# Performance work log

Measured on AMD Instinct MI355X. Metric: run time of the kernel, lower is better.

Reference implementation:

```python
import jax, jax.numpy as jnp
import numpy as np

N, E, D, H = 100000, 1000000, 64, 4
HD = D // H  # head dim
G = 64       # num graphs in batch
EPS = 1e-5
NEG_SLOPE = 0.2


def setup_inputs() -> dict:
    key = jax.random.key(0)
    ks = jax.random.split(key, 10)
    x = jax.random.normal(ks[0], (N, D), dtype=jnp.float32)
    edge_index = jax.random.randint(ks[1], (2, E), 0, N)
    batch = jnp.sort(jax.random.randint(ks[2], (N,), 0, G))
    s = 1.0 / np.sqrt(D)
    Wl = jax.random.uniform(ks[3], (D, D), jnp.float32, -s, s)   # lin_l (source)
    Wr = jax.random.uniform(ks[4], (D, D), jnp.float32, -s, s)   # lin_r (target)
    att = jax.random.uniform(ks[5], (H, HD), jnp.float32, -s, s)
    bias_gat = jnp.zeros((D,), jnp.float32)
    gn_weight = jnp.ones((D,), jnp.float32)
    gn_bias = jnp.zeros((D,), jnp.float32)
    gn_mean_scale = jnp.ones((D,), jnp.float32)
    return {"x": x, "edge_index": edge_index, "batch": batch, "Wl": Wl,
            "Wr": Wr, "att": att, "bias_gat": bias_gat, "gn_weight": gn_weight,
            "gn_bias": gn_bias, "gn_mean_scale": gn_mean_scale}


def _gatv2(x, src, dst, Wl, Wr, att, bias_gat):
    # per-node linear projections, reshaped to heads
    xl = (x @ Wl).reshape(N, H, HD)  # source features
    xr = (x @ Wr).reshape(N, H, HD)  # target features
    # per-edge attention logits: a^T LeakyReLU(xl_j + xr_i)
    e = xl[src] + xr[dst]                             # [E', H, HD]
    e = jnp.where(e >= 0, e, NEG_SLOPE * e)           # leaky_relu
    score = jnp.einsum('ehd,hd->eh', e, att)          # [E', H]
    # segment softmax over incoming edges of each dst node
    m = jax.ops.segment_max(score, dst, num_segments=N)   # [N, H]
    p = jnp.exp(score - m[dst])
    denom = jax.ops.segment_sum(p, dst, num_segments=N)   # [N, H]
    alpha = p / denom[dst]                                # [E', H]
    # weighted scatter-add aggregation of source features
    out = jax.ops.segment_sum(alpha[:, :, None] * xl[src], dst, num_segments=N)
    return out.reshape(N, D) + bias_gat


def _graph_norm(h, batch, weight, bias, mean_scale):
    cnt = jax.ops.segment_sum(jnp.ones((N,), h.dtype), batch, num_segments=G)
    cnt = jnp.maximum(cnt, 1.0)[:, None]                      # [G,1]
    mean = jax.ops.segment_sum(h, batch, num_segments=G) / cnt
    out = h - mean_scale * mean[batch]
    var = jax.ops.segment_sum(out * out, batch, num_segments=G) / cnt
    return weight * out / jnp.sqrt(var[batch] + EPS) + bias


def reference(x, edge_index, batch, Wl, Wr, att, bias_gat, gn_weight, gn_bias, gn_mean_scale):
    # eval mode: dropout / DropEdge are identity; pre_norm=False; res_proj=Identity
    loops = jnp.arange(N)
    src = jnp.concatenate([edge_index[0], loops])  # add self-loops (PyG default)
    dst = jnp.concatenate([edge_index[1], loops])
    h = _gatv2(x, src, dst, Wl, Wr, att, bias_gat)
    h = h + x                                       # identity residual
    h = jnp.where(h > 0, h, jnp.expm1(h))           # ELU
    h = _graph_norm(h, batch, gn_weight, gn_bias, gn_mean_scale)
    return h
```

## Files before the change

kernel.cpp:

```cpp
#include <hip/hip_runtime.h>
#include <hip/hip_bf16.h>
#include <math.h>

#define G_ 64
#define NEG_SLOPE 0.2f
#define EPS_ 1e-5f
#define BBITS 7
#define BSZ 128
#define CAP 2048
#define EPB 2048

typedef __attribute__((ext_vector_type(8))) unsigned short ushort8;
typedef __attribute__((ext_vector_type(8))) short bf16x8;
typedef __attribute__((ext_vector_type(4))) float f32x4;

#define DPP_ADD(t, ctrl)                                                   \
  do {                                                                     \
    int _p = __builtin_amdgcn_update_dpp(0, __float_as_int(t), (ctrl),     \
                                         0xf, 0xf, true);                  \
    (t) += __int_as_float(_p);                                             \
  } while (0)
#define REDUCE8(t)                                                         \
  do {                                                                     \
    DPP_ADD(t, 0xB1);                                                      \
    DPP_ADD(t, 0x4E);                                                      \
    DPP_ADD(t, 0x141);                                                     \
  } while (0)

__device__ __forceinline__ float leaky_(float e) {
  return 0.6f * e + 0.4f * fabsf(e);
}

__device__ __forceinline__ short f2bf(float f) {
  __hip_bfloat16 h = __float2bfloat16(f);
  return *reinterpret_cast<short*>(&h);
}

__global__ __launch_bounds__(256) void init_kernel(
    const float* __restrict__ Wl, const float* __restrict__ Wr,
    bf16x8* __restrict__ bpack, int* __restrict__ bcnt,
    float* __restrict__ gzero, int nb) {
  if (blockIdx.x == 0) {
    const int lane = threadIdx.x;
    if (lane < 64) {
      const int lrow = lane & 15;
      const int lgrp = lane >> 4;
#pragma unroll
      for (int ct = 0; ct < 8; ++ct) {
        const float* W = (ct < 4) ? Wl : Wr;
        const int col = ((ct & 3) * 16) + lrow;
#pragma unroll
        for (int kk = 0; kk < 2; ++kk) {
          const int kb = kk * 32 + lgrp * 8;
          bf16x8 f;
#pragma unroll
          for (int j = 0; j < 8; ++j) f[j] = f2bf(W[(kb + j) * 64 + col]);
          bpack[(ct * 2 + kk) * 64 + lane] = f;
        }
      }
    }
  } else {
    const int idx = (blockIdx.x - 1) * 256 + threadIdx.x;
    const int stride = (gridDim.x - 1) * 256;
    for (int j = idx; j < nb; j += stride) bcnt[j] = 0;
    for (int j = idx; j < 2 * G_ * 64 + G_; j += stride) gzero[j] = 0.f;
  }
}

__global__ __launch_bounds__(256) void projbucket_kernel(
    const float* __restrict__ x, const bf16x8* __restrict__ bpack,
    __hip_bfloat16* __restrict__ xlb, __hip_bfloat16* __restrict__ xrb,
    const int* __restrict__ esrc, const int* __restrict__ edst,
    int* __restrict__ bcnt, unsigned int* __restrict__ packed,
    int n, int e, int nb, int nbucket) {
  __shared__ int cnt[800];
  __shared__ int base[800];
  if ((int)blockIdx.x < nbucket) {
    const int t = threadIdx.x;
    const int e0 = blockIdx.x * EPB;
    const int e1 = (e0 + EPB) < e ? (e0 + EPB) : e;
    int dloc[8], sloc[8];
#pragma unroll
    for (int it = 0; it < 8; ++it) {
      const int i = e0 + t + it * 256;
      const bool ok = i < e1;
      dloc[it] = ok ? edst[i] : -1;
      sloc[it] = ok ? esrc[i] : 0;
    }
    for (int b = t; b < nb; b += 256) cnt[b] = 0;
    __syncthreads();
#pragma unroll
    for (int it = 0; it < 8; ++it)
      if (dloc[it] >= 0) atomicAdd(&cnt[dloc[it] >> BBITS], 1);
    __syncthreads();
    for (int b = t; b < nb; b += 256) {
      int c = cnt[b];
      base[b] = c ? atomicAdd(&bcnt[b], c) : 0;
      cnt[b] = 0;
    }
    __syncthreads();
#pragma unroll
    for (int it = 0; it < 8; ++it) {
      if (dloc[it] >= 0) {
        const int d = dloc[it];
        const int b = d >> BBITS;
        const int pos = base[b] + atomicAdd(&cnt[b], 1);
        if (pos < CAP)
          packed[(size_t)b * CAP + pos] =
              ((unsigned)(d & (BSZ - 1)) << 17) | (unsigned)sloc[it];
      }
    }
  } else {
    const int lane = threadIdx.x & 63;
    const int wv = threadIdx.x >> 6;
    const int rbase = (blockIdx.x - nbucket) * 64 + wv * 16;
    const int lrow = lane & 15;
    const int lgrp = lane >> 4;

    bf16x8 bfrag[8][2];
#pragma unroll
    for (int ct = 0; ct < 8; ++ct)
#pragma unroll
      for (int kk = 0; kk < 2; ++kk)
        bfrag[ct][kk] = bpack[(ct * 2 + kk) * 64 + lane];

    bf16x8 afrag[2];
    const int r = rbase + lrow;
#pragma unroll
    for (int kk = 0; kk < 2; ++kk) {
      bf16x8 f;
      if (r < n) {
        const float4* p =
            (const float4*)(x + (size_t)r * 64 + kk * 32 + lgrp * 8);
        float4 u = p[0], v = p[1];
        f[0] = f2bf(u.x); f[1] = f2bf(u.y); f[2] = f2bf(u.z); f[3] = f2bf(u.w);
        f[4] = f2bf(v.x); f[5] = f2bf(v.y); f[6] = f2bf(v.z); f[7] = f2bf(v.w);
      } else {
        f = bf16x8{0, 0, 0, 0, 0, 0, 0, 0};
      }
      afrag[kk] = f;
    }

    f32x4 acc[8];
#pragma unroll
    for (int ct = 0; ct < 8; ++ct) acc[ct] = f32x4{0.f, 0.f, 0.f, 0.f};
#pragma unroll
    for (int ct = 0; ct < 8; ++ct)
#pragma unroll
      for (int kk = 0; kk < 2; ++kk)
        acc[ct] = __builtin_amdgcn_mfma_f32_16x16x32_bf16(
            afrag[kk], bfrag[ct][kk], acc[ct], 0, 0, 0);

#pragma unroll
    for (int ct = 0; ct < 8; ++ct) {
      __hip_bfloat16* dst = (ct < 4) ? xlb : xrb;
      const int c = ((ct & 3) * 16) + lrow;
#pragma unroll
      for (int j = 0; j < 4; ++j) {
        const int rr = rbase + lgrp * 4 + j;
        if (rr < n) dst[(size_t)rr * 64 + c] = __float2bfloat16(acc[ct][j]);
      }
    }
  }
}

__global__ __launch_bounds__(256) void sort_kernel(
    unsigned int* __restrict__ packed, const int* __restrict__ bcnt,
    int2* __restrict__ nse, int n) {
  __shared__ unsigned int stage[CAP];
  __shared__ int cnt[BSZ];
  __shared__ int sc[BSZ];
  __shared__ int off[BSZ + 1];
  const int t = threadIdx.x;
  const int b = blockIdx.x;
  int ecnt = bcnt[b];
  if (ecnt > CAP) ecnt = CAP;
  for (int j = t; j < ecnt; j += 256) stage[j] = packed[(size_t)b * CAP + j];
  if (t < BSZ) cnt[t] = 0;
  __syncthreads();
  for (int j = t; j < ecnt; j += 256) atomicAdd(&cnt[stage[j] >> 17], 1);
  __syncthreads();
  if (t < BSZ) sc[t] = cnt[t];
  __syncthreads();
#pragma unroll
  for (int o = 1; o < BSZ; o <<= 1) {
    int v = 0;
    if (t < BSZ && t >= o) v = sc[t - o];
    __syncthreads();
    if (t < BSZ) sc[t] += v;
    __syncthreads();
  }
  if (t < BSZ) {
    off[t + 1] = sc[t];
    if (t == 0) off[0] = 0;
    cnt[t] = sc[t] - cnt[t];
  }
  __syncthreads();
  for (int j = t; j < ecnt; j += 256) {
    unsigned v = stage[j];
    int pos = atomicAdd(&cnt[v >> 17], 1);
    packed[(size_t)b * CAP + pos] = v & 0x1FFFF;
  }
  const int nodebase = b << BBITS;
  if (t < BSZ && nodebase + t < n) {
    int s = off[t];
    nse[nodebase + t] = make_int2(b * CAP + s, off[t + 1] - s);
  }
}

template <int NB>
__device__ __forceinline__ void burst_(
    const char* xbase, unsigned poff, int myedge, int half, int tot,
    float xr0, float xr1, float a0, float a1,
    float& acc0, float& acc1, float& den) {
  unsigned vv[NB];
#pragma unroll
  for (int j = 0; j < NB; ++j) {
    const int sa = __builtin_amdgcn_readlane(myedge, 2 * j);
    const int sb = __builtin_amdgcn_readlane(myedge, 2 * j + 1);
    const int s = half ? sb : sa;
    vv[j] = *(const unsigned*)(xbase + (((unsigned)s << 7) | poff));
  }
#pragma unroll
  for (int j = 0; j < NB; ++j) {
    const unsigned v = vv[j];
    const float l0 = __uint_as_float(v << 16);
    const float l1 = __uint_as_float(v & 0xFFFF0000u);
    float e0 = leaky_(l0 + xr0);
    float e1 = leaky_(l1 + xr1);
    float t = a0 * e0 + a1 * e1;
    REDUCE8(t);
    float p = exp2f(t);
    p = ((2 * j + half) < tot) ? p : 0.f;
    acc0 = fmaf(p, l0, acc0);
    acc1 = fmaf(p, l1, acc1);
    den += p;
  }
}

__global__ __launch_bounds__(256) void aggregate_kernel(
    const __hip_bfloat16* __restrict__ xlb,
    const __hip_bfloat16* __restrict__ xrb, const float* __restrict__ x,
    const float* __restrict__ att, const float* __restrict__ bias_gat,
    const int2* __restrict__ nse, const unsigned int* __restrict__ srt,
    __hip_bfloat16* __restrict__ hb, int n) {
  const int lane = threadIdx.x & 63;
  const int i = (blockIdx.x * blockDim.x + threadIdx.x) >> 6;
  if (i >= n) return;
  const int pos = lane & 31;
  const int half = lane >> 5;
  const float2 attp = ((const float2*)att)[pos];
  const float a0 = attp.x * 1.44269504f;
  const float a1 = attp.y * 1.44269504f;
  const unsigned xr_pk = ((const unsigned*)(xrb + (size_t)i * 64))[pos];
  const float xr0 = __uint_as_float(xr_pk << 16);
  const float xr1 = __uint_as_float(xr_pk & 0xFFFF0000u);
  int2 sd = nse[i];
  const int s0 = __builtin_amdgcn_readfirstlane(sd.x);
  const int deg = __builtin_amdgcn_readfirstlane(sd.y);
  const int tot = deg + 1;
  int myedge = i;
  if (lane > 0 && lane < tot) myedge = (int)srt[s0 + lane - 1];
  float acc0 = 0.f, acc1 = 0.f, den = 0.f;
  const char* xbase = (const char*)xlb;
  const unsigned poff = (unsigned)pos << 2;

  if (tot <= 8) {
    burst_<4>(xbase, poff, myedge, half, tot, xr0, xr1, a0, a1,
              acc0, acc1, den);
  } else {
    burst_<8>(xbase, poff, myedge, half, tot, xr0, xr1, a0, a1,
              acc0, acc1, den);
    const int kmax = tot < 64 ? tot : 64;
    for (int k = 16; k < kmax; k += 2) {
      const int sa = __builtin_amdgcn_readlane(myedge, k);
      const int sb = (k + 1 < kmax) ? __builtin_amdgcn_readlane(myedge, k + 1)
                                    : sa;
      const int s = half ? sb : sa;
      const unsigned v = *(const unsigned*)(xbase + (((unsigned)s << 7) | poff));
      const float l0 = __uint_as_float(v << 16);
      const float l1 = __uint_as_float(v & 0xFFFF0000u);
      float e0 = leaky_(l0 + xr0);
      float e1 = leaky_(l1 + xr1);
      float t = a0 * e0 + a1 * e1;
      REDUCE8(t);
      float p = exp2f(t);
      p = ((k + half) < kmax) ? p : 0.f;
      acc0 = fmaf(p, l0, acc0);
      acc1 = fmaf(p, l1, acc1);
      den += p;
    }
    for (int kk = 64; kk < tot; ++kk) {
      const int s = (int)srt[s0 + kk - 1];
      const unsigned v = *(const unsigned*)(xbase + (((unsigned)s << 7) | poff));
      const float l0 = __uint_as_float(v << 16);
      const float l1 = __uint_as_float(v & 0xFFFF0000u);
      float e0 = leaky_(l0 + xr0);
      float e1 = leaky_(l1 + xr1);
      float t = a0 * e0 + a1 * e1;
      REDUCE8(t);
      float p = exp2f(t);
      p = half ? 0.f : p;
      acc0 = fmaf(p, l0, acc0);
      acc1 = fmaf(p, l1, acc1);
      den += p;
    }
  }

  acc0 += __shfl_xor(acc0, 32);
  acc1 += __shfl_xor(acc1, 32);
  den += __shfl_xor(den, 32);
  if (half == 0) {
    const float inv = 1.f / den;
    const float2 xres = ((const float2*)(x + (size_t)i * 64))[pos];
    const float2 bb = ((const float2*)bias_gat)[pos];
    float h0 = fmaf(acc0, inv, bb.x) + xres.x;
    float h1 = fmaf(acc1, inv, bb.y) + xres.y;
    h0 = h0 > 0.f ? h0 : expm1f(h0);
    h1 = h1 > 0.f ? h1 : expm1f(h1);
    __hip_bfloat16 b0 = __float2bfloat16(h0);
    __hip_bfloat16 b1 = __float2bfloat16(h1);
    unsigned pk = ((unsigned)(*(unsigned short*)&b1) << 16) |
                  (unsigned)(*(unsigned short*)&b0);
    ((unsigned*)(hb + (size_t)i * 64))[pos] = pk;
  }
}

__global__ __launch_bounds__(256) void gsum2_kernel(
    const __hip_bfloat16* __restrict__ h, const int* __restrict__ batch,
    float* __restrict__ gsum, float* __restrict__ gsq,
    float* __restrict__ gcnt, int n) {
  const int lane = threadIdx.x & 63;
  const int wave = (blockIdx.x * blockDim.x + threadIdx.x) >> 6;
  const int nwaves = (gridDim.x * blockDim.x) >> 6;
  const int chunk = (n + nwaves - 1) / nwaves;
  const int start = wave * chunk;
  const int end = (start + chunk) < n ? (start + chunk) : n;
  float s1 = 0.f, s2 = 0.f, cntl = 0.f;
  int curg = -1;
  for (int i = start; i < end; ++i) {
    int g = batch[i];
    if (g != curg) {
      if (curg >= 0) {
        atomicAdd(&gsum[curg * 64 + lane], s1);
        atomicAdd(&gsq[curg * 64 + lane], s2);
        if (lane == 0) atomicAdd(&gcnt[curg], cntl);
      }
      curg = g; s1 = 0.f; s2 = 0.f; cntl = 0.f;
    }
    float hv = __bfloat162float(h[(size_t)i * 64 + lane]);
    s1 += hv;
    s2 += hv * hv;
    cntl += 1.f;
  }
  if (curg >= 0) {
    atomicAdd(&gsum[curg * 64 + lane], s1);
    atomicAdd(&gsq[curg * 64 + lane], s2);
    if (lane == 0) atomicAdd(&gcnt[curg], cntl);
  }
}

__global__ __launch_bounds__(256) void out_kernel(
    const __hip_bfloat16* __restrict__ hb, const int* __restrict__ batch,
    const float* __restrict__ gsum, const float* __restrict__ gsq,
    const float* __restrict__ gcnt, const float* __restrict__ mscale,
    const float* __restrict__ w, const float* __restrict__ bias,
    float* __restrict__ out, int n) {
  const int total8 = n * 8;
  for (int idx = blockIdx.x * blockDim.x + threadIdx.x; idx < total8;
       idx += gridDim.x * blockDim.x) {
    int i = idx >> 3, q = idx & 7;
    int g = batch[i];
    float c = gcnt[g];
    c = c > 1.f ? c : 1.f;
    float inv = 1.f / c;
    int base = g * 64 + q * 8;
    ushort8 hv8 = ((const ushort8*)hb)[idx];
    float r[8];
#pragma unroll
    for (int j = 0; j < 8; ++j) {
      int dd = q * 8 + j;
      float mean = gsum[base + j] * inv;
      float ms = mscale[dd];
      float var = gsq[base + j] * inv - ms * (2.f - ms) * mean * mean;
      float f = __uint_as_float(((unsigned)hv8[j]) << 16);
      r[j] = (f - ms * mean) * (w[dd] * rsqrtf(var + EPS_)) + bias[dd];
    }
    float4 o0 = make_float4(r[0], r[1], r[2], r[3]);
    float4 o1 = make_float4(r[4], r[5], r[6], r[7]);
    ((float4*)out)[idx * 2] = o0;
    ((float4*)out)[idx * 2 + 1] = o1;
  }
}

extern "C" void kernel_launch(void* const* d_in, const int* in_sizes, int n_in,
                              void* d_out, int out_size, void* d_ws, size_t ws_size,
                              hipStream_t stream) {
  const float* x        = (const float*)d_in[0];
  const int*   eidx     = (const int*)d_in[1];
  const int*   batch    = (const int*)d_in[2];
  const float* Wl       = (const float*)d_in[3];
  const float* Wr       = (const float*)d_in[4];
  const float* att      = (const float*)d_in[5];
  const float* bias_gat = (const float*)d_in[6];
  const float* gw       = (const float*)d_in[7];
  const float* gb       = (const float*)d_in[8];
  const float* gms      = (const float*)d_in[9];
  const int N = in_sizes[0] / 64;
  const int E = in_sizes[1] / 2;
  const int* esrc = eidx;
  const int* edst = eidx + E;
  float* out = (float*)d_out;
  const int NB_ = (N + BSZ - 1) >> BBITS;

  char* wsp = (char*)d_ws;
  float* gsum   = (float*)wsp;                wsp += G_ * 64 * 4;
  float* gsq    = (float*)wsp;                wsp += G_ * 64 * 4;
  float* gcnt   = (float*)wsp;                wsp += G_ * 4;
  bf16x8* bpack = (bf16x8*)wsp;               wsp += 16 * 64 * 16;
  int*   bcnt   = (int*)wsp;                  wsp += (size_t)NB_ * 4;
  int2*  nse    = (int2*)wsp;                 wsp += (size_t)N * 8;
  unsigned int* packed = (unsigned int*)wsp;  wsp += (size_t)NB_ * CAP * 4;
  __hip_bfloat16* xlb = (__hip_bfloat16*)wsp; wsp += (size_t)N * 64 * 2;
  __hip_bfloat16* xrb = (__hip_bfloat16*)wsp; wsp += (size_t)N * 64 * 2;
  __hip_bfloat16* hb  = (__hip_bfloat16*)wsp; wsp += (size_t)N * 64 * 2;

  init_kernel<<<9, 256, 0, stream>>>(Wl, Wr, bpack, bcnt, gsum, NB_);

  const int nbucket = (E + EPB - 1) / EPB;
  const int nproj = (N + 63) / 64;
  projbucket_kernel<<<nbucket + nproj, 256, 0, stream>>>(
      x, bpack, xlb, xrb, esrc, edst, bcnt, packed, N, E, NB_, nbucket);

  sort_kernel<<<NB_, 256, 0, stream>>>(packed, bcnt, nse, N);

  aggregate_kernel<<<(N + 3) / 4, 256, 0, stream>>>(
      xlb, xrb, x, att, bias_gat, nse, packed, hb, N);

  gsum2_kernel<<<1024, 256, 0, stream>>>(hb, batch, gsum, gsq, gcnt, N);
  out_kernel<<<3125, 256, 0, stream>>>(hb, batch, gsum, gsq, gcnt, gms, gw,
                                       gb, out, N);
}
```

Measured before the change: 153.9 us.

## Pair projection with sort kernel and store bf16 copy of x for residual

The edge-bucketing step becomes its own kernel, and the node projection GEMM now shares a launch with the per-bucket sort kernel instead of the bucketing kernel. This balances work across the two launches. The projection also writes a bf16 copy of x, so the aggregate kernel reads the residual at half the bytes instead of fp32 x. In exchange it adds an extra N×64 bf16 write and workspace buffer, and the residual is rounded to bf16 precision.

```diff
diff --git a/kernel.cpp b/kernel.cpp
--- a/kernel.cpp
+++ b/kernel.cpp
@@ -67,53 +67,98 @@
   }
 }
 
-__global__ __launch_bounds__(256) void projbucket_kernel(
-    const float* __restrict__ x, const bf16x8* __restrict__ bpack,
-    __hip_bfloat16* __restrict__ xlb, __hip_bfloat16* __restrict__ xrb,
+__global__ __launch_bounds__(256) void bucket_kernel(
     const int* __restrict__ esrc, const int* __restrict__ edst,
     int* __restrict__ bcnt, unsigned int* __restrict__ packed,
-    int n, int e, int nb, int nbucket) {
+    int e, int nb) {
   __shared__ int cnt[800];
   __shared__ int base[800];
-  if ((int)blockIdx.x < nbucket) {
+  const int t = threadIdx.x;
+  const int e0 = blockIdx.x * EPB;
+  const int e1 = (e0 + EPB) < e ? (e0 + EPB) : e;
+  int dloc[8], sloc[8];
+#pragma unroll
+  for (int it = 0; it < 8; ++it) {
+    const int i = e0 + t + it * 256;
+    const bool ok = i < e1;
+    dloc[it] = ok ? edst[i] : -1;
+    sloc[it] = ok ? esrc[i] : 0;
+  }
+  for (int b = t; b < nb; b += 256) cnt[b] = 0;
+  __syncthreads();
+#pragma unroll
+  for (int it = 0; it < 8; ++it)
+    if (dloc[it] >= 0) atomicAdd(&cnt[dloc[it] >> BBITS], 1);
+  __syncthreads();
+  for (int b = t; b < nb; b += 256) {
+    int c = cnt[b];
+    base[b] = c ? atomicAdd(&bcnt[b], c) : 0;
+    cnt[b] = 0;
+  }
+  __syncthreads();
+#pragma unroll
+  for (int it = 0; it < 8; ++it) {
+    if (dloc[it] >= 0) {
+      const int d = dloc[it];
+      const int b = d >> BBITS;
+      const int pos = base[b] + atomicAdd(&cnt[b], 1);
+      if (pos < CAP)
+        packed[(size_t)b * CAP + pos] =
+            ((unsigned)(d & (BSZ - 1)) << 17) | (unsigned)sloc[it];
+    }
+  }
+}
+
+__global__ __launch_bounds__(256) void sortproj_kernel(
+    unsigned int* __restrict__ packed, const int* __restrict__ bcnt,
+    int2* __restrict__ nse, const float* __restrict__ x,
+    const bf16x8* __restrict__ bpack, __hip_bfloat16* __restrict__ xlb,
+    __hip_bfloat16* __restrict__ xrb, __hip_bfloat16* __restrict__ xb,
+    int n, int nsort) {
+  __shared__ unsigned int stage[CAP];
+  __shared__ int cnt[BSZ];
+  __shared__ int sc[BSZ];
+  __shared__ int off[BSZ + 1];
+  if ((int)blockIdx.x < nsort) {
     const int t = threadIdx.x;
-    const int e0 = blockIdx.x * EPB;
-    const int e1 = (e0 + EPB) < e ? (e0 + EPB) : e;
-    int dloc[8], sloc[8];
-#pragma unroll
-    for (int it = 0; it < 8; ++it) {
-      const int i = e0 + t + it * 256;
-      const bool ok = i < e1;
-      dloc[it] = ok ? edst[i] : -1;
-      sloc[it] = ok ? esrc[i] : 0;
-    }
-    for (int b = t; b < nb; b += 256) cnt[b] = 0;
+    const int b = blockIdx.x;
+    int ecnt = bcnt[b];
+    if (ecnt > CAP) ecnt = CAP;
+    for (int j = t; j < ecnt; j += 256) stage[j] = packed[(size_t)b * CAP + j];
+    if (t < BSZ) cnt[t] = 0;
     __syncthreads();
-#pragma unroll
-    for (int it = 0; it < 8; ++it)
-      if (dloc[it] >= 0) atomicAdd(&cnt[dloc[it] >> BBITS], 1);
+    for (int j = t; j < ecnt; j += 256) atomicAdd(&cnt[stage[j] >> 17], 1);
     __syncthreads();
-    for (int b = t; b < nb; b += 256) {
-      int c = cnt[b];
-      base[b] = c ? atomicAdd(&bcnt[b], c) : 0;
-      cnt[b] = 0;
-    }
+    if (t < BSZ) sc[t] = cnt[t];
     __syncthreads();
 #pragma unroll
-    for (int it = 0; it < 8; ++it) {
-      if (dloc[it] >= 0) {
-        const int d = dloc[it];
-        const int b = d >> BBITS;
-        const int pos = base[b] + atomicAdd(&cnt[b], 1);
-        if (pos < CAP)
-          packed[(size_t)b * CAP + pos] =
-              ((unsigned)(d & (BSZ - 1)) << 17) | (unsigned)sloc[it];
-      }
+    for (int o = 1; o < BSZ; o <<= 1) {
+      int v = 0;
+      if (t < BSZ && t >= o) v = sc[t - o];
+      __syncthreads();
+      if (t < BSZ) sc[t] += v;
+      __syncthreads();
+    }
+    if (t < BSZ) {
+      off[t + 1] = sc[t];
+      if (t == 0) off[0] = 0;
+      cnt[t] = sc[t] - cnt[t];
+    }
+    __syncthreads();
+    for (int j = t; j < ecnt; j += 256) {
+      unsigned v = stage[j];
+      int pos = atomicAdd(&cnt[v >> 17], 1);
+      packed[(size_t)b * CAP + pos] = v & 0x1FFFF;
+    }
+    const int nodebase = b << BBITS;
+    if (t < BSZ && nodebase + t < n) {
+      int s = off[t];
+      nse[nodebase + t] = make_int2(b * CAP + s, off[t + 1] - s);
     }
   } else {
     const int lane = threadIdx.x & 63;
     const int wv = threadIdx.x >> 6;
-    const int rbase = (blockIdx.x - nbucket) * 64 + wv * 16;
+    const int rbase = (blockIdx.x - nsort) * 64 + wv * 16;
     const int lrow = lane & 15;
     const int lgrp = lane >> 4;
 
@@ -135,6 +180,7 @@
         float4 u = p[0], v = p[1];
         f[0] = f2bf(u.x); f[1] = f2bf(u.y); f[2] = f2bf(u.z); f[3] = f2bf(u.w);
         f[4] = f2bf(v.x); f[5] = f2bf(v.y); f[6] = f2bf(v.z); f[7] = f2bf(v.w);
+        *reinterpret_cast<bf16x8*>(xb + (size_t)r * 64 + kk * 32 + lgrp * 8) = f;
       } else {
         f = bf16x8{0, 0, 0, 0, 0, 0, 0, 0};
       }
@@ -161,50 +207,6 @@
         if (rr < n) dst[(size_t)rr * 64 + c] = __float2bfloat16(acc[ct][j]);
       }
     }
-  }
-}
-
-__global__ __launch_bounds__(256) void sort_kernel(
-    unsigned int* __restrict__ packed, const int* __restrict__ bcnt,
-    int2* __restrict__ nse, int n) {
-  __shared__ unsigned int stage[CAP];
-  __shared__ int cnt[BSZ];
-  __shared__ int sc[BSZ];
-  __shared__ int off[BSZ + 1];
-  const int t = threadIdx.x;
-  const int b = blockIdx.x;
-  int ecnt = bcnt[b];
-  if (ecnt > CAP) ecnt = CAP;
-  for (int j = t; j < ecnt; j += 256) stage[j] = packed[(size_t)b * CAP + j];
-  if (t < BSZ) cnt[t] = 0;
-  __syncthreads();
-  for (int j = t; j < ecnt; j += 256) atomicAdd(&cnt[stage[j] >> 17], 1);
-  __syncthreads();
-  if (t < BSZ) sc[t] = cnt[t];
-  __syncthreads();
-#pragma unroll
-  for (int o = 1; o < BSZ; o <<= 1) {
-    int v = 0;
-    if (t < BSZ && t >= o) v = sc[t - o];
-    __syncthreads();
-    if (t < BSZ) sc[t] += v;
-    __syncthreads();
-  }
-  if (t < BSZ) {
-    off[t + 1] = sc[t];
-    if (t == 0) off[0] = 0;
-    cnt[t] = sc[t] - cnt[t];
-  }
-  __syncthreads();
-  for (int j = t; j < ecnt; j += 256) {
-    unsigned v = stage[j];
-    int pos = atomicAdd(&cnt[v >> 17], 1);
-    packed[(size_t)b * CAP + pos] = v & 0x1FFFF;
-  }
-  const int nodebase = b << BBITS;
-  if (t < BSZ && nodebase + t < n) {
-    int s = off[t];
-    nse[nodebase + t] = make_int2(b * CAP + s, off[t + 1] - s);
   }
 }
 
@@ -240,10 +242,11 @@
 
 __global__ __launch_bounds__(256) void aggregate_kernel(
     const __hip_bfloat16* __restrict__ xlb,
-    const __hip_bfloat16* __restrict__ xrb, const float* __restrict__ x,
-    const float* __restrict__ att, const float* __restrict__ bias_gat,
-    const int2* __restrict__ nse, const unsigned int* __restrict__ srt,
-    __hip_bfloat16* __restrict__ hb, int n) {
+    const __hip_bfloat16* __restrict__ xrb,
+    const __hip_bfloat16* __restrict__ xb, const float* __restrict__ att,
+    const float* __restrict__ bias_gat, const int2* __restrict__ nse,
+    const unsigned int* __restrict__ srt, __hip_bfloat16* __restrict__ hb,
+    int n) {
   const int lane = threadIdx.x & 63;
   const int i = (blockIdx.x * blockDim.x + threadIdx.x) >> 6;
   if (i >= n) return;
@@ -312,10 +315,12 @@
   den += __shfl_xor(den, 32);
   if (half == 0) {
     const float inv = 1.f / den;
-    const float2 xres = ((const float2*)(x + (size_t)i * 64))[pos];
+    const unsigned xpk = ((const unsigned*)(xb + (size_t)i * 64))[pos];
+    const float xres0 = __uint_as_float(xpk << 16);
+    const float xres1 = __uint_as_float(xpk & 0xFFFF0000u);
     const float2 bb = ((const float2*)bias_gat)[pos];
-    float h0 = fmaf(acc0, inv, bb.x) + xres.x;
-    float h1 = fmaf(acc1, inv, bb.y) + xres.y;
+    float h0 = fmaf(acc0, inv, bb.x) + xres0;
+    float h1 = fmaf(acc1, inv, bb.y) + xres1;
     h0 = h0 > 0.f ? h0 : expm1f(h0);
     h1 = h1 > 0.f ? h1 : expm1f(h1);
     __hip_bfloat16 b0 = __float2bfloat16(h0);
@@ -423,19 +428,20 @@
   unsigned int* packed = (unsigned int*)wsp;  wsp += (size_t)NB_ * CAP * 4;
   __hip_bfloat16* xlb = (__hip_bfloat16*)wsp; wsp += (size_t)N * 64 * 2;
   __hip_bfloat16* xrb = (__hip_bfloat16*)wsp; wsp += (size_t)N * 64 * 2;
+  __hip_bfloat16* xb  = (__hip_bfloat16*)wsp; wsp += (size_t)N * 64 * 2;
   __hip_bfloat16* hb  = (__hip_bfloat16*)wsp; wsp += (size_t)N * 64 * 2;
 
   init_kernel<<<9, 256, 0, stream>>>(Wl, Wr, bpack, bcnt, gsum, NB_);
 
   const int nbucket = (E + EPB - 1) / EPB;
+  bucket_kernel<<<nbucket, 256, 0, stream>>>(esrc, edst, bcnt, packed, E, NB_);
+
   const int nproj = (N + 63) / 64;
-  projbucket_kernel<<<nbucket + nproj, 256, 0, stream>>>(
-      x, bpack, xlb, xrb, esrc, edst, bcnt, packed, N, E, NB_, nbucket);
-
-  sort_kernel<<<NB_, 256, 0, stream>>>(packed, bcnt, nse, N);
+  sortproj_kernel<<<NB_ + nproj, 256, 0, stream>>>(
+      packed, bcnt, nse, x, bpack, xlb, xrb, xb, N, NB_);
 
   aggregate_kernel<<<(N + 3) / 4, 256, 0, stream>>>(
-      xlb, xrb, x, att, bias_gat, nse, packed, hb, N);
+      xlb, xrb, xb, att, bias_gat, nse, packed, hb, N);
 
   gsum2_kernel<<<1024, 256, 0, stream>>>(hb, batch, gsum, gsq, gcnt, N);
   out_kernel<<<3125, 256, 0, stream>>>(hb, batch, gsum, gsq, gcnt, gms, gw,
```

After: 150.6 us. 1.02x faster.
